# Kernel optimization log

Measured on AMD Instinct MI355X. Metric: run time of the kernel, lower is better.

The kernel has to match this reference:

```python
import jax, jax.numpy as jnp
import numpy as np

NUM_LAYERS = 4
D_MODEL = 512
D_INNER = 1024   # 2 * d_model (Mamba expand=2)
D_STATE = 16
DT_RANK = 32     # ceil(d_model / 16)
D_CONV = 4
BATCH = 2
SEQ = 512
EPS = 1e-5


def _rmsnorm(x, w, eps=EPS):
    # fused add+RMSNorm math: fp32 reduction, scale by weight (no bias)
    x = x.astype(jnp.float32)
    return x * jax.lax.rsqrt(jnp.mean(x * x, axis=-1, keepdims=True) + eps) * w


def _silu(x):
    return x * jax.nn.sigmoid(x)


def _causal_conv(x, w, b):
    # x: (B, D, L); w: (D, K) depthwise causal conv, left-pad K-1, take first L
    xp = jnp.pad(x, ((0, 0), (0, 0), (D_CONV - 1, 0)))
    out = jax.lax.conv_general_dilated(
        xp, w[:, None, :], (1,), 'VALID',
        dimension_numbers=('NCH', 'OIH', 'NCH'),
        feature_group_count=x.shape[1])
    return out + b[None, :, None]


def _selective_scan(u, delta, A, Bm, Cm):
    # u, delta: (B, D, L); A: (D, N); Bm, Cm: (B, N, L)
    xs = (jnp.moveaxis(delta, 2, 0), jnp.moveaxis(u, 2, 0),
          jnp.moveaxis(Bm, 2, 0), jnp.moveaxis(Cm, 2, 0))
    h0 = jnp.zeros((u.shape[0], u.shape[1], A.shape[1]), u.dtype)

    def step(h, xst):
        d_t, u_t, b_t, c_t = xst                     # (B,D),(B,D),(B,N),(B,N)
        dA = jnp.exp(d_t[:, :, None] * A[None])      # (B,D,N) ZOH discretization
        h = h * dA + (d_t * u_t)[:, :, None] * b_t[:, None, :]
        y = jnp.einsum('bdn,bn->bd', h, c_t)
        return h, y

    _, ys = jax.lax.scan(step, h0, xs)
    return jnp.moveaxis(ys, 0, 2)                    # (B, D, L)


def _ssm_branch(x, z, cw, cb, xpw, dtw, dtb, Alog, Dskip):
    x = _silu(_causal_conv(x, cw, cb))                              # (B, Din, L)
    x_dbl = jnp.einsum('rd,bdl->brl', xpw, x)                       # (B, R+2N, L)
    dt, Bm, Cm = jnp.split(x_dbl, [DT_RANK, DT_RANK + D_STATE], axis=1)
    delta = jax.nn.softplus(jnp.einsum('dr,brl->bdl', dtw, dt) + dtb[None, :, None])
    A = -jnp.exp(Alog.astype(jnp.float32))                          # (Din, N)
    y = _selective_scan(x, delta, A, Bm, Cm)
    y = y + Dskip[None, :, None] * x
    return y * _silu(z)


def _encoder(x, norm_w, in_proj_w, convw_f, convb_f, xpw_f, dtw_f, dtb_f,
             Alog_f, Dskip_f, convw_r, convb_r, xpw_r, dtw_r, dtb_r,
             Alog_r, Dskip_r, out_proj_w, normf_w):
    residual = None
    hs = x
    feats = []
    for i in range(NUM_LAYERS):
        # fused add + RMSNorm, prenorm=True, residual_in_fp32
        residual = hs if residual is None else (hs + residual)
        residual = residual.astype(jnp.float32)
        hn = _rmsnorm(residual, norm_w[i])
        # bimamba v2 mixer
        xz = jnp.einsum('ed,bld->bel', in_proj_w[i], hn)            # (B, 2Din, L)
        xi, zi = jnp.split(xz, 2, axis=1)
        y_f = _ssm_branch(xi, zi, convw_f[i], convb_f[i], xpw_f[i], dtw_f[i],
                          dtb_f[i], Alog_f[i], Dskip_f[i])
        y_r = _ssm_branch(xi[:, :, ::-1], zi[:, :, ::-1], convw_r[i], convb_r[i],
                          xpw_r[i], dtw_r[i], dtb_r[i], Alog_r[i], Dskip_r[i])
        y = y_f + y_r[:, :, ::-1]
        hs = jnp.einsum('bel,de->bld', y, out_proj_w[i])
        feats.append(hs)
    out = _rmsnorm(hs + residual, normf_w)                          # prenorm=False
    return out, feats


def setup_inputs() -> dict:
    key = jax.random.key(0)
    ks = jax.random.split(key, 12)
    Ly = NUM_LAYERS
    s = 0.02

    def nrm(k, shape):
        return jax.random.normal(k, shape, jnp.float32) * s

    dt = 1e-3 + jax.random.uniform(ks[11], (Ly, D_INNER), jnp.float32) * (0.1 - 1e-3)
    dtb = jnp.log(jnp.expm1(dt))  # inverse softplus of dt init
    Alog = jnp.log(jnp.broadcast_to(
        jnp.arange(1, D_STATE + 1, dtype=jnp.float32), (Ly, D_INNER, D_STATE)))
    return dict(
        x=jax.random.normal(ks[0], (BATCH, SEQ, D_MODEL), jnp.float32),
        norm_w=jnp.ones((Ly, D_MODEL), jnp.float32),
        in_proj_w=nrm(ks[1], (Ly, 2 * D_INNER, D_MODEL)),
        convw_f=nrm(ks[2], (Ly, D_INNER, D_CONV)),
        convb_f=jnp.zeros((Ly, D_INNER), jnp.float32),
        xpw_f=nrm(ks[3], (Ly, DT_RANK + 2 * D_STATE, D_INNER)),
        dtw_f=nrm(ks[4], (Ly, D_INNER, DT_RANK)),
        dtb_f=dtb,
        Alog_f=Alog,
        Dskip_f=jnp.ones((Ly, D_INNER), jnp.float32),
        convw_r=nrm(ks[5], (Ly, D_INNER, D_CONV)),
        convb_r=jnp.zeros((Ly, D_INNER), jnp.float32),
        xpw_r=nrm(ks[6], (Ly, DT_RANK + 2 * D_STATE, D_INNER)),
        dtw_r=nrm(ks[7], (Ly, D_INNER, DT_RANK)),
        dtb_r=dtb,
        Alog_r=Alog,
        Dskip_r=jnp.ones((Ly, D_INNER), jnp.float32),
        out_proj_w=nrm(ks[8], (Ly, D_MODEL, D_INNER)),
        normf_w=jnp.ones((D_MODEL,), jnp.float32),
    )


def reference(x, norm_w, in_proj_w, convw_f, convb_f, xpw_f, dtw_f, dtb_f,
              Alog_f, Dskip_f, convw_r, convb_r, xpw_r, dtw_r, dtb_r,
              Alog_r, Dskip_r, out_proj_w, normf_w):
    out, feats = _encoder(x, norm_w, in_proj_w, convw_f, convb_f, xpw_f, dtw_f,
                          dtb_f, Alog_f, Dskip_f, convw_r, convb_r, xpw_r,
                          dtw_r, dtb_r, Alog_r, Dskip_r, out_proj_w, normf_w)
    return (out, jnp.stack(feats))
```

## Files before the change

kernel.cpp:

```cpp
#include <hip/hip_runtime.h>

#define BATCH 2
#define SEQ 512
#define DMODEL 512
#define DINNER 1024
#define DSTATE 16
#define DTRANK 32
#define NBL (BATCH*SEQ)
#define EPSV 1e-5f

typedef __attribute__((ext_vector_type(8))) short bf16x8;
typedef __attribute__((ext_vector_type(4))) float f32x4;

static __device__ __forceinline__ float sigmoidf_(float x) {
  return 1.0f / (1.0f + __expf(-x));
}
static __device__ __forceinline__ float softplusf_(float x) {
  return fmaxf(x, 0.0f) + log1pf(__expf(-fabsf(x)));
}
static __device__ __forceinline__ unsigned short f2bf(float x) {
  unsigned int u = __float_as_uint(x);
  unsigned int r = (u + 0x7FFFu + ((u >> 16) & 1u)) >> 16;
  return (unsigned short)r;
}

__global__ __launch_bounds__(256) void wconvert_kernel(
    const float* __restrict__ s0, const float* __restrict__ s1,
    const float* __restrict__ s2, const float* __restrict__ s3,
    const float* __restrict__ s4, const float* __restrict__ s5,
    unsigned short* __restrict__ d0, unsigned short* __restrict__ d1,
    unsigned short* __restrict__ d2, unsigned short* __restrict__ d3,
    unsigned short* __restrict__ d4, unsigned short* __restrict__ d5) {
  long i = (long)(blockIdx.x * 256 + threadIdx.x) * 8;
  const float* src; unsigned short* dst;
  if (i < 4194304)      { src = s0; dst = d0; }
  else if (i < 6291456) { src = s1; dst = d1; i -= 4194304; }
  else if (i < 6553600) { src = s2; dst = d2; i -= 6291456; }
  else if (i < 6815744) { src = s3; dst = d3; i -= 6553600; }
  else if (i < 6946816) { src = s4; dst = d4; i -= 6815744; }
  else                  { src = s5; dst = d5; i -= 6946816; }
  const float4 v0 = *(const float4*)&src[i];
  const float4 v1 = *(const float4*)&src[i + 4];
  bf16x8 o;
  o[0] = (short)f2bf(v0.x); o[1] = (short)f2bf(v0.y);
  o[2] = (short)f2bf(v0.z); o[3] = (short)f2bf(v0.w);
  o[4] = (short)f2bf(v1.x); o[5] = (short)f2bf(v1.y);
  o[6] = (short)f2bf(v1.z); o[7] = (short)f2bf(v1.w);
  *(bf16x8*)&dst[i] = o;
}

__global__ __launch_bounds__(256) void addnorm_kernel(
    const float* __restrict__ hs, float* __restrict__ residual,
    const float* __restrict__ w, float* __restrict__ out,
    unsigned short* __restrict__ outb, int first) {
  const int row = blockIdx.x;
  const int t = threadIdx.x;
  const float* hp = hs + (long)row * DMODEL;
  float* rp = residual + (long)row * DMODEL;
  float r0 = hp[t], r1 = hp[t + 256];
  if (!first) { r0 += rp[t]; r1 += rp[t + 256]; }
  rp[t] = r0; rp[t + 256] = r1;
  float ss = r0 * r0 + r1 * r1;
  #pragma unroll
  for (int off = 32; off; off >>= 1) ss += __shfl_xor(ss, off, 64);
  __shared__ float sw[4];
  const int wid = t >> 6, lane = t & 63;
  if (lane == 0) sw[wid] = ss;
  __syncthreads();
  const float tot = sw[0] + sw[1] + sw[2] + sw[3];
  const float scale = rsqrtf(tot * (1.0f / (float)DMODEL) + EPSV);
  const float v0 = r0 * scale * w[t];
  const float v1 = r1 * scale * w[t + 256];
  if (out) {
    out[(long)row * DMODEL + t] = v0;
    out[(long)row * DMODEL + t + 256] = v1;
  }
  if (outb) {
    outb[(long)row * DMODEL + t] = f2bf(v0);
    outb[(long)row * DMODEL + t + 256] = f2bf(v1);
  }
}

#define LDK 40
#define LDK2 72

__global__ __launch_bounds__(256) void gemm_in_kernel(
    const unsigned short* __restrict__ A, const unsigned short* __restrict__ B,
    float* __restrict__ C) {
  __shared__ unsigned short As[128 * LDK2];
  __shared__ unsigned short Bs[64 * LDK2];
  const int t = threadIdx.x;
  const int m0 = blockIdx.y * 128, n0 = blockIdx.x * 64;
  const int lane = t & 63;
  const int w = t >> 6;
  const int wr = (w >> 1) * 64, wc = (w & 1) * 32;
  const int fr = lane & 15;
  const int fq = lane >> 4;
  const int K = DMODEL;

  f32x4 acc[4][2];
  #pragma unroll
  for (int i = 0; i < 4; ++i)
    #pragma unroll
    for (int j = 0; j < 2; ++j) {
      f32x4 z = {0.f, 0.f, 0.f, 0.f};
      acc[i][j] = z;
    }

  const int arow = t >> 1, ako = (t & 1) * 32;
  const int brow = t >> 2, bko = (t & 3) * 16;

  bf16x8 pa[4], pb[2];
  #define LOADG_IN(k0_) do {                                              \
    const unsigned short* ap = &A[(long)(m0 + arow) * K + (k0_) + ako];   \
    pa[0] = *(const bf16x8*)ap;        pa[1] = *(const bf16x8*)(ap + 8);  \
    pa[2] = *(const bf16x8*)(ap + 16); pa[3] = *(const bf16x8*)(ap + 24); \
    const unsigned short* bp = &B[(long)(n0 + brow) * K + (k0_) + bko];   \
    pb[0] = *(const bf16x8*)bp;        pb[1] = *(const bf16x8*)(bp + 8);  \
  } while (0)

  LOADG_IN(0);
  for (int k0 = 0; k0 < K; k0 += 64) {
    if (k0) __syncthreads();
    *(bf16x8*)&As[arow * LDK2 + ako]      = pa[0];
    *(bf16x8*)&As[arow * LDK2 + ako + 8]  = pa[1];
    *(bf16x8*)&As[arow * LDK2 + ako + 16] = pa[2];
    *(bf16x8*)&As[arow * LDK2 + ako + 24] = pa[3];
    *(bf16x8*)&Bs[brow * LDK2 + bko]      = pb[0];
    *(bf16x8*)&Bs[brow * LDK2 + bko + 8]  = pb[1];
    __syncthreads();
    if (k0 + 64 < K) LOADG_IN(k0 + 64);
    #pragma unroll
    for (int h = 0; h < 2; ++h) {
      bf16x8 af[4], bg[2];
      #pragma unroll
      for (int i = 0; i < 4; ++i)
        af[i] = *(const bf16x8*)&As[(wr + i * 16 + fr) * LDK2 + h * 32 + fq * 8];
      #pragma unroll
      for (int j = 0; j < 2; ++j)
        bg[j] = *(const bf16x8*)&Bs[(wc + j * 16 + fr) * LDK2 + h * 32 + fq * 8];
      #pragma unroll
      for (int i = 0; i < 4; ++i)
        #pragma unroll
        for (int j = 0; j < 2; ++j)
          acc[i][j] = __builtin_amdgcn_mfma_f32_16x16x32_bf16(
              af[i], bg[j], acc[i][j], 0, 0, 0);
    }
  }
  #undef LOADG_IN

  #pragma unroll
  for (int i = 0; i < 4; ++i)
    #pragma unroll
    for (int j = 0; j < 2; ++j)
      #pragma unroll
      for (int r2 = 0; r2 < 4; ++r2) {
        const int m = m0 + wr + i * 16 + fq * 4 + r2;
        const int n = n0 + wc + j * 16 + fr;
        C[(long)m * NBL + n] = acc[i][j][r2];
      }
}

__global__ __launch_bounds__(256) void conv_silu_kernel(
    const float* __restrict__ xz,
    const float* __restrict__ cw_f, const float* __restrict__ cb_f,
    const float* __restrict__ cw_r, const float* __restrict__ cb_r,
    float* __restrict__ xconv_f, float* __restrict__ xconv_r,
    unsigned short* __restrict__ xcT) {
  __shared__ unsigned short tile[32][33];
  const int dir = blockIdx.z;
  const int n0 = blockIdx.x * 32, d0 = blockIdx.y * 32;
  const int b = n0 >> 9;
  const int l0 = n0 & (SEQ - 1);
  const float* cw = dir ? cw_r : cw_f;
  const float* cb = dir ? cb_r : cb_f;
  float* xconv = dir ? xconv_r : xconv_f;
  unsigned short* dst = xcT + (long)dir * DINNER * NBL;
  const int t = threadIdx.x;
  const int c = t & 31, rr = t >> 5;
  #pragma unroll
  for (int p = 0; p < 4; ++p) {
    const int d = d0 + p * 8 + rr;
    const int l = l0 + c;
    const float* xi = xz + (long)d * NBL + b * SEQ;
    float sum = cb[d];
    #pragma unroll
    for (int k = 0; k < 4; ++k) {
      const int tt = l - 3 + k;
      if (tt >= 0) {
        const int src = dir ? (SEQ - 1 - tt) : tt;
        sum += cw[d * 4 + k] * xi[src];
      }
    }
    const float v = sum * sigmoidf_(sum);
    xconv[(long)d * NBL + n0 + c] = v;
    tile[p * 8 + rr][c] = f2bf(v);
  }
  __syncthreads();
  #pragma unroll
  for (int p = 0; p < 4; ++p) {
    const int n = n0 + p * 8 + rr;
    dst[(long)n * DINNER + d0 + c] = tile[c][p * 8 + rr];
  }
}

__global__ __launch_bounds__(256) void xdbl_mfma_kernel(
    const unsigned short* __restrict__ xpwb_f, const unsigned short* __restrict__ xpwb_r,
    const unsigned short* __restrict__ xcT,
    unsigned short* __restrict__ dtT,
    float* __restrict__ xbc_f, float* __restrict__ xbc_r) {
  __shared__ unsigned short As[64 * LDK2];
  __shared__ unsigned short Bs[128 * LDK2];
  const int t = threadIdx.x;
  const int dir = blockIdx.y;
  const int n0 = blockIdx.x * 128;
  const unsigned short* A = dir ? xpwb_r : xpwb_f;
  const unsigned short* B = xcT + (long)dir * DINNER * NBL;
  float* xbc = dir ? xbc_r : xbc_f;
  unsigned short* dtt = dtT + (long)dir * NBL * DTRANK;

  const int lane = t & 63;
  const int w = t >> 6;
  const int fr = lane & 15;
  const int fq = lane >> 4;

  f32x4 acc[4][2];
  #pragma unroll
  for (int i = 0; i < 4; ++i)
    #pragma unroll
    for (int j = 0; j < 2; ++j) {
      f32x4 z = {0.f, 0.f, 0.f, 0.f};
      acc[i][j] = z;
    }

  const int arow = t >> 2, ako = (t & 3) * 16;
  const int brow = t >> 1, bko = (t & 1) * 32;

  bf16x8 pa[2], pb[4];
  #define LOADG_XD(k0_) do {                                                   \
    const unsigned short* ap = &A[(long)arow * DINNER + (k0_) + ako];          \
    pa[0] = *(const bf16x8*)ap;        pa[1] = *(const bf16x8*)(ap + 8);       \
    const unsigned short* bp = &B[(long)(n0 + brow) * DINNER + (k0_) + bko];   \
    pb[0] = *(const bf16x8*)bp;        pb[1] = *(const bf16x8*)(bp + 8);       \
    pb[2] = *(const bf16x8*)(bp + 16); pb[3] = *(const bf16x8*)(bp + 24);      \
  } while (0)

  LOADG_XD(0);
  for (int k0 = 0; k0 < DINNER; k0 += 64) {
    if (k0) __syncthreads();
    *(bf16x8*)&As[arow * LDK2 + ako]      = pa[0];
    *(bf16x8*)&As[arow * LDK2 + ako + 8]  = pa[1];
    *(bf16x8*)&Bs[brow * LDK2 + bko]      = pb[0];
    *(bf16x8*)&Bs[brow * LDK2 + bko + 8]  = pb[1];
    *(bf16x8*)&Bs[brow * LDK2 + bko + 16] = pb[2];
    *(bf16x8*)&Bs[brow * LDK2 + bko + 24] = pb[3];
    __syncthreads();
    if (k0 + 64 < DINNER) LOADG_XD(k0 + 64);
    #pragma unroll
    for (int h = 0; h < 2; ++h) {
      bf16x8 af[4], bg[2];
      #pragma unroll
      for (int i = 0; i < 4; ++i)
        af[i] = *(const bf16x8*)&As[(i * 16 + fr) * LDK2 + h * 32 + fq * 8];
      #pragma unroll
      for (int j = 0; j < 2; ++j)
        bg[j] = *(const bf16x8*)&Bs[(w * 32 + j * 16 + fr) * LDK2 + h * 32 + fq * 8];
      #pragma unroll
      for (int i = 0; i < 4; ++i)
        #pragma unroll
        for (int j = 0; j < 2; ++j)
          acc[i][j] = __builtin_amdgcn_mfma_f32_16x16x32_bf16(
              af[i], bg[j], acc[i][j], 0, 0, 0);
    }
  }
  #undef LOADG_XD

  #pragma unroll
  for (int i = 0; i < 4; ++i)
    #pragma unroll
    for (int j = 0; j < 2; ++j)
      #pragma unroll
      for (int r2 = 0; r2 < 4; ++r2) {
        const int m = i * 16 + fq * 4 + r2;
        const int n = n0 + w * 32 + j * 16 + fr;
        const float v = acc[i][j][r2];
        if (m < DTRANK) dtt[(long)n * DTRANK + m] = f2bf(v);
        else xbc[(long)(m - 32) * NBL + n] = v;
      }
}

__global__ __launch_bounds__(256) void deltam_kernel(
    const unsigned short* __restrict__ dtwb_f, const unsigned short* __restrict__ dtwb_r,
    const unsigned short* __restrict__ dtT,
    const float* __restrict__ dtb_f, const float* __restrict__ dtb_r,
    float* __restrict__ delta_f, float* __restrict__ delta_r) {
  __shared__ unsigned short As[128 * LDK];
  __shared__ unsigned short Bs[128 * LDK];
  const int t = threadIdx.x;
  const int dir = blockIdx.z;
  const unsigned short* A = dir ? dtwb_r : dtwb_f;
  const unsigned short* B = dtT + (long)dir * NBL * DTRANK;
  const float* dtb = dir ? dtb_r : dtb_f;
  float* dl = dir ? delta_r : delta_f;
  const int m0 = blockIdx.y * 128, n0 = blockIdx.x * 128;
  const int lane = t & 63;
  const int w = t >> 6;
  const int wr = (w >> 1) * 64, wc = (w & 1) * 64;
  const int fr = lane & 15;
  const int fq = lane >> 4;

  const int srow = t >> 1;
  const int sko = (t & 1) * 16;
  *(bf16x8*)&As[srow * LDK + sko] =
      *(const bf16x8*)&A[(long)(m0 + srow) * DTRANK + sko];
  *(bf16x8*)&As[srow * LDK + sko + 8] =
      *(const bf16x8*)&A[(long)(m0 + srow) * DTRANK + sko + 8];
  *(bf16x8*)&Bs[srow * LDK + sko] =
      *(const bf16x8*)&B[(long)(n0 + srow) * DTRANK + sko];
  *(bf16x8*)&Bs[srow * LDK + sko + 8] =
      *(const bf16x8*)&B[(long)(n0 + srow) * DTRANK + sko + 8];
  __syncthreads();

  bf16x8 af[4], bg[4];
  #pragma unroll
  for (int i = 0; i < 4; ++i) {
    af[i] = *(const bf16x8*)&As[(wr + i * 16 + fr) * LDK + fq * 8];
    bg[i] = *(const bf16x8*)&Bs[(wc + i * 16 + fr) * LDK + fq * 8];
  }
  f32x4 acc[4][4];
  #pragma unroll
  for (int i = 0; i < 4; ++i)
    #pragma unroll
    for (int j = 0; j < 4; ++j) {
      f32x4 z = {0.f, 0.f, 0.f, 0.f};
      acc[i][j] = __builtin_amdgcn_mfma_f32_16x16x32_bf16(af[i], bg[j], z, 0, 0, 0);
    }

  #pragma unroll
  for (int i = 0; i < 4; ++i) {
    const int m = m0 + wr + i * 16 + fq * 4;
    #pragma unroll
    for (int r2 = 0; r2 < 4; ++r2) {
      const float bias = dtb[m + r2];
      #pragma unroll
      for (int j = 0; j < 4; ++j) {
        const int n = n0 + wc + j * 16 + fr;
        dl[(long)(m + r2) * NBL + n] = softplusf_(acc[i][j][r2] + bias);
      }
    }
  }
}

static __device__ __forceinline__ void scan_pass(
    const float* __restrict__ dp, const float* __restrict__ up,
    const float* __restrict__ bct, const float* __restrict__ Alog,
    float Dv, int lane, float out[8], float u[8]) {
  float dt[8], dtu[8];
  {
    const float4 a0 = *(const float4*)&dp[0];
    const float4 a1 = *(const float4*)&dp[4];
    dt[0] = a0.x; dt[1] = a0.y; dt[2] = a0.z; dt[3] = a0.w;
    dt[4] = a1.x; dt[5] = a1.y; dt[6] = a1.z; dt[7] = a1.w;
    const float4 b0 = *(const float4*)&up[0];
    const float4 b1 = *(const float4*)&up[4];
    u[0] = b0.x; u[1] = b0.y; u[2] = b0.z; u[3] = b0.w;
    u[4] = b1.x; u[5] = b1.y; u[6] = b1.z; u[7] = b1.w;
  }
  #pragma unroll
  for (int j = 0; j < 8; ++j) { dtu[j] = dt[j] * u[j]; out[j] = 0.f; }

  for (int n = 0; n < DSTATE; ++n) {
    const float An = -__expf(Alog[n]);
    float Bv[8], Cv[8], dA[8], cB[8];
    {
      const float* bp = bct + (long)n * NBL;
      const float* cp = bct + (long)(DSTATE + n) * NBL;
      const float4 b0 = *(const float4*)&bp[0];
      const float4 b1 = *(const float4*)&bp[4];
      Bv[0] = b0.x; Bv[1] = b0.y; Bv[2] = b0.z; Bv[3] = b0.w;
      Bv[4] = b1.x; Bv[5] = b1.y; Bv[6] = b1.z; Bv[7] = b1.w;
      const float4 c0 = *(const float4*)&cp[0];
      const float4 c1 = *(const float4*)&cp[4];
      Cv[0] = c0.x; Cv[1] = c0.y; Cv[2] = c0.z; Cv[3] = c0.w;
      Cv[4] = c1.x; Cv[5] = c1.y; Cv[6] = c1.z; Cv[7] = c1.w;
    }
    float h = 0.f, P = 1.f;
    #pragma unroll
    for (int j = 0; j < 8; ++j) {
      dA[j] = __expf(dt[j] * An);
      cB[j] = dtu[j] * Bv[j];
      h = fmaf(h, dA[j], cB[j]);
      P *= dA[j];
    }
    float hs = h, Ps = P;
    #pragma unroll
    for (int off = 1; off < 64; off <<= 1) {
      const float hp = __shfl_up(hs, off, 64);
      const float Pp = __shfl_up(Ps, off, 64);
      if (lane >= off) { hs = fmaf(hp, Ps, hs); Ps *= Pp; }
    }
    float h0 = __shfl_up(hs, 1, 64);
    if (lane == 0) h0 = 0.f;
    #pragma unroll
    for (int j = 0; j < 8; ++j) {
      h0 = fmaf(h0, dA[j], cB[j]);
      out[j] = fmaf(h0, Cv[j], out[j]);
    }
  }
  #pragma unroll
  for (int j = 0; j < 8; ++j) out[j] = fmaf(Dv, u[j], out[j]);
}

__global__ __launch_bounds__(256) void scan_merged_kernel(
    const float* __restrict__ delta_f, const float* __restrict__ delta_r,
    const float* __restrict__ xconv_f, const float* __restrict__ xconv_r,
    const float* __restrict__ xbc_f, const float* __restrict__ xbc_r,
    const float* __restrict__ Alog_f, const float* __restrict__ Alog_r,
    const float* __restrict__ Dsk_f, const float* __restrict__ Dsk_r,
    const float* __restrict__ xz, float* __restrict__ y) {
  const int t = threadIdx.x;
  const int wv = t >> 6;
  const int lane = t & 63;
  const int row = blockIdx.x * 4 + wv;
  const int b = row >> 10, d = row & 1023;
  const long rbase = (long)d * NBL + b * SEQ;

  float af[8], ar[8], uf[8], ur[8];
  scan_pass(delta_f + rbase + lane * 8, xconv_f + rbase + lane * 8,
            xbc_f + b * SEQ + lane * 8, Alog_f + d * DSTATE,
            Dsk_f[d], lane, af, uf);
  scan_pass(delta_r + rbase + lane * 8, xconv_r + rbase + lane * 8,
            xbc_r + b * SEQ + lane * 8, Alog_r + d * DSTATE,
            Dsk_r[d], lane, ar, ur);

  const float* zp = xz + (long)(DINNER + d) * NBL + b * SEQ + lane * 8;
  float* yp = y + rbase + lane * 8;
  const float4 z0 = *(const float4*)&zp[0];
  const float4 z1 = *(const float4*)&zp[4];
  const float zv[8] = {z0.x, z0.y, z0.z, z0.w, z1.x, z1.y, z1.z, z1.w};
  float out[8];
  #pragma unroll
  for (int j = 0; j < 8; ++j) {
    const float v = __shfl(ar[7 - j], 63 - lane, 64);
    out[j] = (af[j] + v) * (zv[j] * sigmoidf_(zv[j]));
  }
  float4 o0 = {out[0], out[1], out[2], out[3]};
  float4 o1 = {out[4], out[5], out[6], out[7]};
  *(float4*)&yp[0] = o0;
  *(float4*)&yp[4] = o1;
}

__global__ __launch_bounds__(256) void ytrans_kernel(
    const float* __restrict__ yf, unsigned short* __restrict__ yt) {
  __shared__ unsigned short tile[32][33];
  const int e0 = blockIdx.y * 32, n0 = blockIdx.x * 32;
  const int t = threadIdx.x;
  const int c = t & 31, r8 = t >> 5;
  #pragma unroll
  for (int p = 0; p < 4; ++p) {
    const int e = e0 + p * 8 + r8;
    tile[p * 8 + r8][c] = f2bf(yf[(long)e * NBL + n0 + c]);
  }
  __syncthreads();
  #pragma unroll
  for (int p = 0; p < 4; ++p) {
    const int n = n0 + p * 8 + r8;
    yt[(long)n * DINNER + e0 + c] = tile[c][p * 8 + r8];
  }
}

__global__ __launch_bounds__(256) void gemm_out_kernel(
    const unsigned short* __restrict__ A, const unsigned short* __restrict__ B,
    float* __restrict__ C) {
  __shared__ unsigned short As[128 * LDK2];
  __shared__ unsigned short Bs[128 * LDK2];
  const int t = threadIdx.x;
  const int m0 = blockIdx.y * 128, n0 = blockIdx.x * 128;
  const int lane = t & 63;
  const int w = t >> 6;
  const int wr = (w >> 1) * 64, wc = (w & 1) * 64;
  const int fr = lane & 15;
  const int fq = lane >> 4;
  const int K = DINNER;

  f32x4 acc[4][4];
  #pragma unroll
  for (int i = 0; i < 4; ++i)
    #pragma unroll
    for (int j = 0; j < 4; ++j) {
      f32x4 z = {0.f, 0.f, 0.f, 0.f};
      acc[i][j] = z;
    }

  const int srow = t >> 1, sko = (t & 1) * 32;

  bf16x8 pa[4], pb[4];
  #define LOADG_OUT(k0_) do {                                              \
    const unsigned short* ap = &A[(long)(m0 + srow) * K + (k0_) + sko];    \
    pa[0] = *(const bf16x8*)ap;        pa[1] = *(const bf16x8*)(ap + 8);   \
    pa[2] = *(const bf16x8*)(ap + 16); pa[3] = *(const bf16x8*)(ap + 24);  \
    const unsigned short* bp = &B[(long)(n0 + srow) * K + (k0_) + sko];    \
    pb[0] = *(const bf16x8*)bp;        pb[1] = *(const bf16x8*)(bp + 8);   \
    pb[2] = *(const bf16x8*)(bp + 16); pb[3] = *(const bf16x8*)(bp + 24);  \
  } while (0)

  LOADG_OUT(0);
  for (int k0 = 0; k0 < K; k0 += 64) {
    if (k0) __syncthreads();
    *(bf16x8*)&As[srow * LDK2 + sko]      = pa[0];
    *(bf16x8*)&As[srow * LDK2 + sko + 8]  = pa[1];
    *(bf16x8*)&As[srow * LDK2 + sko + 16] = pa[2];
    *(bf16x8*)&As[srow * LDK2 + sko + 24] = pa[3];
    *(bf16x8*)&Bs[srow * LDK2 + sko]      = pb[0];
    *(bf16x8*)&Bs[srow * LDK2 + sko + 8]  = pb[1];
    *(bf16x8*)&Bs[srow * LDK2 + sko + 16] = pb[2];
    *(bf16x8*)&Bs[srow * LDK2 + sko + 24] = pb[3];
    __syncthreads();
    if (k0 + 64 < K) LOADG_OUT(k0 + 64);
    #pragma unroll
    for (int h = 0; h < 2; ++h) {
      bf16x8 af[4], bg[4];
      #pragma unroll
      for (int i = 0; i < 4; ++i) {
        af[i] = *(const bf16x8*)&As[(wr + i * 16 + fr) * LDK2 + h * 32 + fq * 8];
        bg[i] = *(const bf16x8*)&Bs[(wc + i * 16 + fr) * LDK2 + h * 32 + fq * 8];
      }
      #pragma unroll
      for (int i = 0; i < 4; ++i)
        #pragma unroll
        for (int j = 0; j < 4; ++j)
          acc[i][j] = __builtin_amdgcn_mfma_f32_16x16x32_bf16(
              af[i], bg[j], acc[i][j], 0, 0, 0);
    }
  }
  #undef LOADG_OUT

  #pragma unroll
  for (int i = 0; i < 4; ++i)
    #pragma unroll
    for (int j = 0; j < 4; ++j)
      #pragma unroll
      for (int r2 = 0; r2 < 4; ++r2) {
        const int m = m0 + wr + i * 16 + fq * 4 + r2;
        const int n = n0 + wc + j * 16 + fr;
        C[(long)n * DMODEL + m] = acc[i][j][r2];
      }
}

extern "C" void kernel_launch(void* const* d_in, const int* in_sizes, int n_in,
                              void* d_out, int out_size, void* d_ws, size_t ws_size,
                              hipStream_t stream) {
  (void)in_sizes; (void)n_in; (void)out_size; (void)ws_size;
  const float* x       = (const float*)d_in[0];
  const float* norm_w  = (const float*)d_in[1];
  const float* in_proj = (const float*)d_in[2];
  const float* convw_f = (const float*)d_in[3];
  const float* convb_f = (const float*)d_in[4];
  const float* xpw_f   = (const float*)d_in[5];
  const float* dtw_f   = (const float*)d_in[6];
  const float* dtb_f   = (const float*)d_in[7];
  const float* Alog_f  = (const float*)d_in[8];
  const float* Dsk_f   = (const float*)d_in[9];
  const float* convw_r = (const float*)d_in[10];
  const float* convb_r = (const float*)d_in[11];
  const float* xpw_r   = (const float*)d_in[12];
  const float* dtw_r   = (const float*)d_in[13];
  const float* dtb_r   = (const float*)d_in[14];
  const float* Alog_r  = (const float*)d_in[15];
  const float* Dsk_r   = (const float*)d_in[16];
  const float* out_w   = (const float*)d_in[17];
  const float* normf_w = (const float*)d_in[18];

  float* ws = (float*)d_ws;
  float* residual = ws;  ws += 524288;
  float* xzbuf    = ws;  ws += 2097152;
  float* xconv_f  = ws;  ws += 1048576;
  float* xconv_r  = ws;  ws += 1048576;
  float* xbc_f    = ws;  ws += 32768;
  float* xbc_r    = ws;  ws += 32768;
  float* delta_f  = ws;  ws += 1048576;
  float* delta_r  = ws;  ws += 1048576;
  float* ybuf     = ws;  ws += 1048576;
  float* hnb_f    = ws;  ws += 262144;
  float* wbfin_f  = ws;  ws += 2097152;
  float* wbfout_f = ws;  ws += 1048576;
  float* ybt_f    = ws;  ws += 524288;
  float* xcT_f    = ws;  ws += 1048576;
  float* dtT_f    = ws;  ws += 32768;
  float* xpwb_f_  = ws;  ws += 131072;
  float* xpwb_r_  = ws;  ws += 131072;
  float* dtwb_f_  = ws;  ws += 65536;
  float* dtwb_r_  = ws;  ws += 65536;

  unsigned short* hnb = (unsigned short*)hnb_f;
  unsigned short* wbfin = (unsigned short*)wbfin_f;
  unsigned short* wbfout = (unsigned short*)wbfout_f;
  unsigned short* ybt = (unsigned short*)ybt_f;
  unsigned short* xcT = (unsigned short*)xcT_f;
  unsigned short* dtT = (unsigned short*)dtT_f;
  unsigned short* xpwb_f = (unsigned short*)xpwb_f_;
  unsigned short* xpwb_r = (unsigned short*)xpwb_r_;
  unsigned short* dtwb_f = (unsigned short*)dtwb_f_;
  unsigned short* dtwb_r = (unsigned short*)dtwb_r_;

  float* outp = (float*)d_out;

  wconvert_kernel<<<3456, 256, 0, stream>>>(
      in_proj, out_w, xpw_f, xpw_r, dtw_f, dtw_r,
      wbfin, wbfout, xpwb_f, xpwb_r, dtwb_f, dtwb_r);

  for (int layer = 0; layer < 4; ++layer) {
    const float* hsrc = layer == 0 ? x : (outp + (long)layer * 524288);
    addnorm_kernel<<<1024, 256, 0, stream>>>(
        hsrc, residual, norm_w + layer * DMODEL, nullptr, hnb, layer == 0 ? 1 : 0);
    gemm_in_kernel<<<dim3(16, 16), 256, 0, stream>>>(
        wbfin + (long)layer * 2048 * 512, hnb, xzbuf);
    conv_silu_kernel<<<dim3(32, 32, 2), 256, 0, stream>>>(
        xzbuf, convw_f + layer * DINNER * 4, convb_f + layer * DINNER,
        convw_r + layer * DINNER * 4, convb_r + layer * DINNER,
        xconv_f, xconv_r, xcT);
    xdbl_mfma_kernel<<<dim3(8, 2), 256, 0, stream>>>(
        xpwb_f + (long)layer * 64 * DINNER, xpwb_r + (long)layer * 64 * DINNER,
        xcT, dtT, xbc_f, xbc_r);
    deltam_kernel<<<dim3(8, 8, 2), 256, 0, stream>>>(
        dtwb_f + (long)layer * DINNER * DTRANK, dtwb_r + (long)layer * DINNER * DTRANK,
        dtT, dtb_f + layer * DINNER, dtb_r + layer * DINNER, delta_f, delta_r);
    scan_merged_kernel<<<512, 256, 0, stream>>>(
        delta_f, delta_r, xconv_f, xconv_r, xbc_f, xbc_r,
        Alog_f + layer * DINNER * DSTATE, Alog_r + layer * DINNER * DSTATE,
        Dsk_f + layer * DINNER, Dsk_r + layer * DINNER,
        xzbuf, ybuf);
    ytrans_kernel<<<dim3(32, 32), 256, 0, stream>>>(ybuf, ybt);
    gemm_out_kernel<<<dim3(8, 4), 256, 0, stream>>>(
        wbfout + (long)layer * 512 * 1024, ybt,
        outp + (long)(1 + layer) * 524288);
  }
  addnorm_kernel<<<1024, 256, 0, stream>>>(
      outp + 4 * 524288, residual, normf_w, outp, nullptr, 0);
}
```

Measured before the change: 390.1 us.

## Recompute conv+SiLU inside scan and fuse output transpose to bf16

The scan kernel now reads the raw x half of xz and recomputes the depthwise causal conv and SiLU in registers for both directions, using wave shuffles for the halo and the reversal. This drops the fp32 xconv_f/xconv_r writes from conv_silu and their reads in the scan. The scan also writes its gated output directly as transposed bf16 through a small shared-memory tile, which removes the fp32 y buffer and the separate ytrans kernel launch. In exchange the scan kernel does some extra arithmetic and shuffles, and its final stores are scattered 8-byte writes.

```diff
diff --git a/kernel.cpp b/kernel.cpp
--- a/kernel.cpp
+++ b/kernel.cpp
@@ -165,7 +165,6 @@
     const float* __restrict__ xz,
     const float* __restrict__ cw_f, const float* __restrict__ cb_f,
     const float* __restrict__ cw_r, const float* __restrict__ cb_r,
-    float* __restrict__ xconv_f, float* __restrict__ xconv_r,
     unsigned short* __restrict__ xcT) {
   __shared__ unsigned short tile[32][33];
   const int dir = blockIdx.z;
@@ -174,7 +173,6 @@
   const int l0 = n0 & (SEQ - 1);
   const float* cw = dir ? cw_r : cw_f;
   const float* cb = dir ? cb_r : cb_f;
-  float* xconv = dir ? xconv_r : xconv_f;
   unsigned short* dst = xcT + (long)dir * DINNER * NBL;
   const int t = threadIdx.x;
   const int c = t & 31, rr = t >> 5;
@@ -193,7 +191,6 @@
       }
     }
     const float v = sum * sigmoidf_(sum);
-    xconv[(long)d * NBL + n0 + c] = v;
     tile[p * 8 + rr][c] = f2bf(v);
   }
   __syncthreads();
@@ -352,19 +349,15 @@
 }
 
 static __device__ __forceinline__ void scan_pass(
-    const float* __restrict__ dp, const float* __restrict__ up,
+    const float* __restrict__ dp, const float u[8],
     const float* __restrict__ bct, const float* __restrict__ Alog,
-    float Dv, int lane, float out[8], float u[8]) {
+    float Dv, int lane, float out[8]) {
   float dt[8], dtu[8];
   {
     const float4 a0 = *(const float4*)&dp[0];
     const float4 a1 = *(const float4*)&dp[4];
     dt[0] = a0.x; dt[1] = a0.y; dt[2] = a0.z; dt[3] = a0.w;
     dt[4] = a1.x; dt[5] = a1.y; dt[6] = a1.z; dt[7] = a1.w;
-    const float4 b0 = *(const float4*)&up[0];
-    const float4 b1 = *(const float4*)&up[4];
-    u[0] = b0.x; u[1] = b0.y; u[2] = b0.z; u[3] = b0.w;
-    u[4] = b1.x; u[5] = b1.y; u[6] = b1.z; u[7] = b1.w;
   }
   #pragma unroll
   for (int j = 0; j < 8; ++j) { dtu[j] = dt[j] * u[j]; out[j] = 0.f; }
@@ -413,11 +406,13 @@
 
 __global__ __launch_bounds__(256) void scan_merged_kernel(
     const float* __restrict__ delta_f, const float* __restrict__ delta_r,
-    const float* __restrict__ xconv_f, const float* __restrict__ xconv_r,
     const float* __restrict__ xbc_f, const float* __restrict__ xbc_r,
     const float* __restrict__ Alog_f, const float* __restrict__ Alog_r,
     const float* __restrict__ Dsk_f, const float* __restrict__ Dsk_r,
-    const float* __restrict__ xz, float* __restrict__ y) {
+    const float* __restrict__ cw_f, const float* __restrict__ cb_f,
+    const float* __restrict__ cw_r, const float* __restrict__ cb_r,
+    const float* __restrict__ xz, unsigned short* __restrict__ ybt) {
+  __shared__ unsigned short s_t[4][512];
   const int t = threadIdx.x;
   const int wv = t >> 6;
   const int lane = t & 63;
@@ -425,47 +420,86 @@
   const int b = row >> 10, d = row & 1023;
   const long rbase = (long)d * NBL + b * SEQ;
 
-  float af[8], ar[8], uf[8], ur[8];
-  scan_pass(delta_f + rbase + lane * 8, xconv_f + rbase + lane * 8,
-            xbc_f + b * SEQ + lane * 8, Alog_f + d * DSTATE,
-            Dsk_f[d], lane, af, uf);
-  scan_pass(delta_r + rbase + lane * 8, xconv_r + rbase + lane * 8,
-            xbc_r + b * SEQ + lane * 8, Alog_r + d * DSTATE,
-            Dsk_r[d], lane, ar, ur);
+  float xv[8];
+  {
+    const float* xp = xz + rbase + lane * 8;
+    const float4 a0 = *(const float4*)&xp[0];
+    const float4 a1 = *(const float4*)&xp[4];
+    xv[0] = a0.x; xv[1] = a0.y; xv[2] = a0.z; xv[3] = a0.w;
+    xv[4] = a1.x; xv[5] = a1.y; xv[6] = a1.z; xv[7] = a1.w;
+  }
+  float uf[8];
+  {
+    float cw0 = cw_f[d * 4], cw1 = cw_f[d * 4 + 1], cw2 = cw_f[d * 4 + 2],
+          cw3 = cw_f[d * 4 + 3], cb = cb_f[d];
+    float xm1 = __shfl_up(xv[7], 1, 64);
+    float xm2 = __shfl_up(xv[6], 1, 64);
+    float xm3 = __shfl_up(xv[5], 1, 64);
+    const float ext[3] = {xm3, xm2, xm1};
+    #pragma unroll
+    for (int j = 0; j < 8; ++j) {
+      float s = cb + cw3 * xv[j];
+      const int p = lane * 8 + j;
+      #pragma unroll
+      for (int k = 0; k < 3; ++k) {
+        const int idx = j - 3 + k;
+        const float xval = (idx >= 0) ? xv[idx] : ext[3 + idx];
+        if (p - 3 + k >= 0) s += (k == 0 ? cw0 : (k == 1 ? cw1 : cw2)) * xval;
+      }
+      uf[j] = s * sigmoidf_(s);
+    }
+  }
+  float xr[8];
+  #pragma unroll
+  for (int j = 0; j < 8; ++j) xr[j] = __shfl(xv[7 - j], 63 - lane, 64);
+  float ur[8];
+  {
+    float cw0 = cw_r[d * 4], cw1 = cw_r[d * 4 + 1], cw2 = cw_r[d * 4 + 2],
+          cw3 = cw_r[d * 4 + 3], cb = cb_r[d];
+    float xm1 = __shfl_up(xr[7], 1, 64);
+    float xm2 = __shfl_up(xr[6], 1, 64);
+    float xm3 = __shfl_up(xr[5], 1, 64);
+    const float ext[3] = {xm3, xm2, xm1};
+    #pragma unroll
+    for (int j = 0; j < 8; ++j) {
+      float s = cb + cw3 * xr[j];
+      const int p = lane * 8 + j;
+      #pragma unroll
+      for (int k = 0; k < 3; ++k) {
+        const int idx = j - 3 + k;
+        const float xval = (idx >= 0) ? xr[idx] : ext[3 + idx];
+        if (p - 3 + k >= 0) s += (k == 0 ? cw0 : (k == 1 ? cw1 : cw2)) * xval;
+      }
+      ur[j] = s * sigmoidf_(s);
+    }
+  }
+
+  float af[8], ar[8];
+  scan_pass(delta_f + rbase + lane * 8, uf,
+            xbc_f + b * SEQ + lane * 8, Alog_f + d * DSTATE, Dsk_f[d], lane, af);
+  scan_pass(delta_r + rbase + lane * 8, ur,
+            xbc_r + b * SEQ + lane * 8, Alog_r + d * DSTATE, Dsk_r[d], lane, ar);
 
   const float* zp = xz + (long)(DINNER + d) * NBL + b * SEQ + lane * 8;
-  float* yp = y + rbase + lane * 8;
   const float4 z0 = *(const float4*)&zp[0];
   const float4 z1 = *(const float4*)&zp[4];
   const float zv[8] = {z0.x, z0.y, z0.z, z0.w, z1.x, z1.y, z1.z, z1.w};
-  float out[8];
+  bf16x8 obf;
   #pragma unroll
   for (int j = 0; j < 8; ++j) {
     const float v = __shfl(ar[7 - j], 63 - lane, 64);
-    out[j] = (af[j] + v) * (zv[j] * sigmoidf_(zv[j]));
-  }
-  float4 o0 = {out[0], out[1], out[2], out[3]};
-  float4 o1 = {out[4], out[5], out[6], out[7]};
-  *(float4*)&yp[0] = o0;
-  *(float4*)&yp[4] = o1;
-}
-
-__global__ __launch_bounds__(256) void ytrans_kernel(
-    const float* __restrict__ yf, unsigned short* __restrict__ yt) {
-  __shared__ unsigned short tile[32][33];
-  const int e0 = blockIdx.y * 32, n0 = blockIdx.x * 32;
-  const int t = threadIdx.x;
-  const int c = t & 31, r8 = t >> 5;
-  #pragma unroll
-  for (int p = 0; p < 4; ++p) {
-    const int e = e0 + p * 8 + r8;
-    tile[p * 8 + r8][c] = f2bf(yf[(long)e * NBL + n0 + c]);
-  }
+    obf[j] = (short)f2bf((af[j] + v) * (zv[j] * sigmoidf_(zv[j])));
+  }
+  *(bf16x8*)&s_t[wv][lane * 8] = obf;
   __syncthreads();
-  #pragma unroll
-  for (int p = 0; p < 4; ++p) {
-    const int n = n0 + p * 8 + r8;
-    yt[(long)n * DINNER + e0 + c] = tile[c][p * 8 + r8];
+  const int d0 = (blockIdx.x * 4) & 1023;
+  const int bb = (blockIdx.x * 4) >> 10;
+  unsigned short* yrow = ybt + (long)(bb * SEQ) * DINNER + d0;
+  #pragma unroll
+  for (int q = 0; q < 2; ++q) {
+    const int n = t * 2 + q;
+    ushort4 v = {s_t[0][n], s_t[1][n], s_t[2][n], s_t[3][n]};
+    *(ushort4*)&yrow[(long)n * DINNER] = v;
   }
 }
 
@@ -574,13 +608,10 @@
   float* ws = (float*)d_ws;
   float* residual = ws;  ws += 524288;
   float* xzbuf    = ws;  ws += 2097152;
-  float* xconv_f  = ws;  ws += 1048576;
-  float* xconv_r  = ws;  ws += 1048576;
   float* xbc_f    = ws;  ws += 32768;
   float* xbc_r    = ws;  ws += 32768;
   float* delta_f  = ws;  ws += 1048576;
   float* delta_r  = ws;  ws += 1048576;
-  float* ybuf     = ws;  ws += 1048576;
   float* hnb_f    = ws;  ws += 262144;
   float* wbfin_f  = ws;  ws += 2097152;
   float* wbfout_f = ws;  ws += 1048576;
@@ -617,8 +648,7 @@
         wbfin + (long)layer * 2048 * 512, hnb, xzbuf);
     conv_silu_kernel<<<dim3(32, 32, 2), 256, 0, stream>>>(
         xzbuf, convw_f + layer * DINNER * 4, convb_f + layer * DINNER,
-        convw_r + layer * DINNER * 4, convb_r + layer * DINNER,
-        xconv_f, xconv_r, xcT);
+        convw_r + layer * DINNER * 4, convb_r + layer * DINNER, xcT);
     xdbl_mfma_kernel<<<dim3(8, 2), 256, 0, stream>>>(
         xpwb_f + (long)layer * 64 * DINNER, xpwb_r + (long)layer * 64 * DINNER,
         xcT, dtT, xbc_f, xbc_r);
@@ -626,11 +656,12 @@
         dtwb_f + (long)layer * DINNER * DTRANK, dtwb_r + (long)layer * DINNER * DTRANK,
         dtT, dtb_f + layer * DINNER, dtb_r + layer * DINNER, delta_f, delta_r);
     scan_merged_kernel<<<512, 256, 0, stream>>>(
-        delta_f, delta_r, xconv_f, xconv_r, xbc_f, xbc_r,
+        delta_f, delta_r, xbc_f, xbc_r,
         Alog_f + layer * DINNER * DSTATE, Alog_r + layer * DINNER * DSTATE,
         Dsk_f + layer * DINNER, Dsk_r + layer * DINNER,
-        xzbuf, ybuf);
-    ytrans_kernel<<<dim3(32, 32), 256, 0, stream>>>(ybuf, ybt);
+        convw_f + layer * DINNER * 4, convb_f + layer * DINNER,
+        convw_r + layer * DINNER * 4, convb_r + layer * DINNER,
+        xzbuf, ybt);
     gemm_out_kernel<<<dim3(8, 4), 256, 0, stream>>>(
         wbfout + (long)layer * 512 * 1024, ybt,
         outp + (long)(1 + layer) * 524288);
```

Measured after the change: 389.9 us. No clear change (-0.1%).
